# Optimization experiments

Hardware: AMD Instinct MI355X
Metric: run time of the kernel (lower is better)

The kernel has to match this reference:

```python
import jax, jax.numpy as jnp
import numpy as np

HEADS = 8
DIM_HEAD = 64
WINDOW = 128
PERSIST = 4
EPS = 1.1920929e-07  # torch nn.RMSNorm default eps = finfo(fp32).eps


def _rope_freqs(n, d, dtype):
    inv_freq = 1.0 / (10000.0 ** (jnp.arange(0, d, 2, dtype=jnp.float32) / d))
    freqs = jnp.arange(n, dtype=jnp.float32)[:, None] * inv_freq[None, :]  # [n, d/2]
    freqs = jnp.repeat(freqs, 2, axis=-1)  # interleaved repeat -> [n, d]
    return jnp.cos(freqs).astype(dtype), jnp.sin(freqs).astype(dtype)


def _rotate_half(x):
    # interleaved pairs (x0,x1),(x2,x3)... -> (-x1,x0),(-x3,x2)...
    x = x.reshape(*x.shape[:-1], -1, 2)
    x1, x2 = x[..., 0], x[..., 1]
    return jnp.stack((-x2, x1), axis=-1).reshape(*x.shape[:-2], -1)


def setup_inputs() -> dict:
    key = jax.random.key(0)
    k1, k2, k3 = jax.random.split(key, 3)
    B, N, D = 1, 4096, 1024
    dim_inner = HEADS * DIM_HEAD  # 512
    return {
        "seq": jax.random.normal(k1, (B, N, D), dtype=jnp.float32),
        "g": jnp.ones((D,), dtype=jnp.float32),
        "w_qkv": jax.random.normal(k2, (D, 3 * dim_inner), dtype=jnp.float32) * 0.02,
        "w_out": jax.random.normal(k3, (dim_inner, D), dtype=jnp.float32) * 0.02,
    }


def reference(seq, g, w_qkv, w_out):
    B, N, D = seq.shape
    H, Dh = HEADS, DIM_HEAD

    # RMSNorm
    x = seq * jax.lax.rsqrt(jnp.mean(seq * seq, axis=-1, keepdims=True) + EPS) * g

    # QKV projection -> [B, H, N, Dh]
    qkv = x @ w_qkv
    q, k, v = jnp.split(qkv, 3, axis=-1)
    to_heads = lambda t: t.reshape(B, N, H, Dh).transpose(0, 2, 1, 3)
    q, k, v = map(to_heads, (q, k, v))

    # rotary embeddings (same positions for q and k)
    cos, sin = _rope_freqs(N, Dh, q.dtype)
    q = q * cos + _rotate_half(q) * sin
    k = k * cos + _rotate_half(k) * sin

    # causal & (persist | sliding-window) mask
    idx = jnp.arange(N)
    dist = idx[:, None] - idx[None, :]
    mask = (dist >= 0) & ((idx[None, :] < PERSIST) | (dist <= WINDOW))  # [N, N]

    scale = Dh ** -0.5
    scores = jnp.einsum("bhid,bhjd->bhij", q, k) * scale
    neg = -jnp.finfo(scores.dtype).max
    scores = jnp.where(mask[None, None], scores, neg)
    attn = jax.nn.softmax(scores, axis=-1)
    out = jnp.einsum("bhij,bhjd->bhid", attn, v)

    out = out.transpose(0, 2, 1, 3).reshape(B, N, H * Dh)
    return out @ w_out
```

## Files before the change

kernel.cpp:

```cpp
#include <hip/hip_runtime.h>
#include <hip/hip_bf16.h>
#include <math.h>

#define SEQ    4096
#define DMODEL 1024
#define NHEADS 8
#define DH     64
#define DINNER 512
#define NQKV   1536
#define WINDOW 128
#define PERSIST 4
#define EPS 1.1920929e-07f

typedef unsigned short u16;
typedef unsigned int   u32;
typedef __bf16  bf16_8 __attribute__((ext_vector_type(8)));
typedef float   f32x4  __attribute__((ext_vector_type(4)));

union BV { bf16_8 v; u16 s[8]; };

__device__ __forceinline__ float b2f(u16 u) {
    union { u32 i; float f; } v; v.i = ((u32)u) << 16; return v.f;
}
__device__ __forceinline__ u16 f2b(float f) {
    union { float f; u32 i; } v; v.f = f;
    u32 i = v.i;
    u32 r = (i + 0x7fffu + ((i >> 16) & 1u)) >> 16;
    return (u16)r;
}

#define GLD16(gp, lp) __builtin_amdgcn_global_load_lds( \
    (const __attribute__((address_space(1))) void*)(gp), \
    (__attribute__((address_space(3))) void*)(lp), 16, 0, 0)

__device__ __forceinline__ void transpose_tile(const float* __restrict__ src,
                                               u16* __restrict__ dst,
                                               int K, int N, int bn, int bk,
                                               u16 (*t)[65], int tid) {
    int r = tid >> 4, c4 = (tid & 15) * 4;
    #pragma unroll
    for (int it = 0; it < 4; it++) {
        int row = r + it * 16;
        float4 v = *(const float4*)(src + (size_t)(bk + row) * N + bn + c4);
        t[row][c4 + 0] = f2b(v.x);
        t[row][c4 + 1] = f2b(v.y);
        t[row][c4 + 2] = f2b(v.z);
        t[row][c4 + 3] = f2b(v.w);
    }
    __syncthreads();
    #pragma unroll
    for (int it = 0; it < 4; it++) {
        int n = r + it * 16;
        u16* d = dst + (size_t)(bn + n) * K + bk + c4;
        d[0] = t[c4 + 0][n];
        d[1] = t[c4 + 1][n];
        d[2] = t[c4 + 2][n];
        d[3] = t[c4 + 3][n];
    }
}

__global__ __launch_bounds__(256) void prep_kernel(const float* __restrict__ wqkv,
                                                   const float* __restrict__ wout,
                                                   const float* __restrict__ seq,
                                                   const float* __restrict__ g,
                                                   u16* __restrict__ wqkv_bt,
                                                   u16* __restrict__ wout_bt,
                                                   u16* __restrict__ x) {
    __shared__ u16 t[64][65];
    __shared__ float wsum[4];
    int b = blockIdx.x, tid = threadIdx.x;
    if (b < 384) {
        transpose_tile(wqkv, wqkv_bt, DMODEL, NQKV, (b % 24) * 64, (b / 24) * 64, t, tid);
    } else if (b < 512) {
        int bb = b - 384;
        transpose_tile(wout, wout_bt, DINNER, DMODEL, (bb % 16) * 64, (bb / 16) * 64, t, tid);
    } else {
        int row = b - 512;
        float4 v = *(const float4*)(seq + (size_t)row * DMODEL + tid * 4);
        float ss = v.x*v.x + v.y*v.y + v.z*v.z + v.w*v.w;
        #pragma unroll
        for (int o = 32; o > 0; o >>= 1) ss += __shfl_xor(ss, o);
        if ((tid & 63) == 0) wsum[tid >> 6] = ss;
        __syncthreads();
        float tot = wsum[0] + wsum[1] + wsum[2] + wsum[3];
        float rstd = rsqrtf(tot * (1.0f / DMODEL) + EPS);
        float4 gv = *(const float4*)(g + tid * 4);
        uint2 o;
        o.x = (u32)f2b(v.x * rstd * gv.x) | ((u32)f2b(v.y * rstd * gv.y) << 16);
        o.y = (u32)f2b(v.z * rstd * gv.z) | ((u32)f2b(v.w * rstd * gv.w) << 16);
        *(uint2*)(x + (size_t)row * DMODEL + tid * 4) = o;
    }
}

template <int MODE>
__global__ __launch_bounds__(256, 2) void gemm2_kernel(const u16* __restrict__ A,
                                                       const u16* __restrict__ Bt,
                                                       u16* __restrict__ C0,
                                                       u16* __restrict__ C1,
                                                       u16* __restrict__ C2,
                                                       float* __restrict__ Cf,
                                                       int M, int N, int K) {
    __shared__ u16 As[128 * 64];
    __shared__ u16 Bs[128 * 64];
    int bx = blockIdx.x, by = blockIdx.y, tid = threadIdx.x;
    int lane = tid & 63, wave = tid >> 6;
    int m16 = lane & 15, quad = lane >> 4;
    int rw0 = (wave & 1) * 64, cw0 = (wave >> 1) * 64;

    f32x4 acc[4][4];
    #pragma unroll
    for (int mt = 0; mt < 4; mt++)
        #pragma unroll
        for (int nt = 0; nt < 4; nt++) acc[mt][nt] = (f32x4){0.f, 0.f, 0.f, 0.f};

    int lrow = lane & 7, lkc = lane >> 3;
    const u16* Ag = A  + (size_t)(by * 128 + lrow) * K + lkc * 8;
    const u16* Bg = Bt + (size_t)(bx * 128 + lrow) * K + lkc * 8;

    for (int k0 = 0; k0 < K; k0 += 64) {
        #pragma unroll
        for (int r = 0; r < 4; r++) {
            int gg = wave * 4 + r;
            GLD16(Ag + (size_t)(gg * 8) * K + k0, As + gg * 512);
            GLD16(Bg + (size_t)(gg * 8) * K + k0, Bs + gg * 512);
        }
        __syncthreads();

        #pragma unroll
        for (int kk = 0; kk < 2; kk++) {
            int kc = kk * 4 + quad;
            bf16_8 afr[4], bfr[4];
            #pragma unroll
            for (int mt = 0; mt < 4; mt++) {
                int row = rw0 + mt * 16 + m16;
                afr[mt] = *(const bf16_8*)(As + (row >> 3) * 512 + kc * 64 + (row & 7) * 8);
            }
            #pragma unroll
            for (int nt = 0; nt < 4; nt++) {
                int col = cw0 + nt * 16 + m16;
                bfr[nt] = *(const bf16_8*)(Bs + (col >> 3) * 512 + kc * 64 + (col & 7) * 8);
            }
            #pragma unroll
            for (int mt = 0; mt < 4; mt++)
                #pragma unroll
                for (int nt = 0; nt < 4; nt++)
                    acc[mt][nt] = __builtin_amdgcn_mfma_f32_16x16x32_bf16(afr[mt], bfr[nt], acc[mt][nt], 0, 0, 0);
        }
        __syncthreads();
    }

    #pragma unroll
    for (int nt = 0; nt < 4; nt++) {
        int col = bx * 128 + cw0 + nt * 16 + m16;
        if (MODE == 0) {
            int tt = (col & 63) >> 1;
            float inv = exp2f(-(float)(2 * tt) * (13.287712379549449f / 64.0f));
            bool isv = (col >= 2 * DINNER);
            bool odd = (col & 1);
            int tens = col >> 9, hh = (col >> 6) & 7, dh = col & 63;
            u16* dst = (tens == 0) ? C0 : ((tens == 1) ? C1 : C2);
            #pragma unroll
            for (int mt = 0; mt < 4; mt++) {
                #pragma unroll
                for (int r = 0; r < 4; r++) {
                    int row = by * 128 + rw0 + mt * 16 + quad * 4 + r;
                    float own = acc[mt][nt][r];
                    float part = __shfl_xor(own, 1);
                    float val = own;
                    if (!isv) {
                        float s, c;
                        __sincosf((float)row * inv, &s, &c);
                        val = odd ? (own * c + part * s) : (own * c - part * s);
                    }
                    dst[((size_t)hh * SEQ + row) * DH + dh] = f2b(val);
                }
            }
        } else {
            #pragma unroll
            for (int mt = 0; mt < 4; mt++) {
                #pragma unroll
                for (int r = 0; r < 4; r++) {
                    int row = by * 128 + rw0 + mt * 16 + quad * 4 + r;
                    Cf[(size_t)row * N + col] = acc[mt][nt][r];
                }
            }
        }
    }
}

#define AROWS 208
#define KLD   72
#define PLD   168
#define VLD   222

__global__ __launch_bounds__(256, 2) void attn_mfma(const u16* __restrict__ Q,
                                                    const u16* __restrict__ Kt,
                                                    const u16* __restrict__ V,
                                                    u16* __restrict__ O) {
    __shared__ __align__(16) char smem[29952 + 64 * VLD * 2];
    u16* Ks = (u16*)smem;
    u16* Ps = (u16*)smem;
    u16* Vt = (u16*)(smem + 29952);
    int i0 = blockIdx.x * 64, h = blockIdx.y;
    int tid = threadIdx.x, wave = tid >> 6, lane = tid & 63;
    int m16 = lane & 15, quad = lane >> 4;
    int smin = (i0 > WINDOW) ? i0 - WINDOW : 0;

    for (int idx = tid; idx < AROWS * 8; idx += 256) {
        int row = idx >> 3, c = idx & 7;
        int j = (row < 16) ? row : (smin + row - 16);
        size_t goff = ((size_t)h * SEQ + j) * DH + c * 8;
        *(bf16_8*)(Ks + row * KLD + c * 8) = *(const bf16_8*)(Kt + goff);
        union BV u; u.v = *(const bf16_8*)(V + goff);
        #pragma unroll
        for (int e = 0; e < 8; e++) Vt[(c * 8 + e) * VLD + row] = u.s[e];
    }

    int iw0 = i0 + wave * 16;
    int iq = iw0 + m16;
    const u16* qrow = Q + ((size_t)h * SEQ + iq) * DH;
    bf16_8 qa = *(const bf16_8*)(qrow + quad * 8);
    bf16_8 qb = *(const bf16_8*)(qrow + 32 + quad * 8);
    __syncthreads();

    int start_w = (iw0 > WINDOW) ? iw0 - WINDOW : 0;
    int Dw = start_w - smin;
    int tlast = 31 + iw0 - start_w;
    int nch = (tlast >> 4) + 1;
    int nk32 = (tlast >> 5) + 1;

    f32x4 S[10];
    #pragma unroll
    for (int c = 0; c < 10; c++) {
        if (c < nch) {
            int t = c * 16 + m16;
            int row = (c == 0) ? t : (t + Dw);
            const u16* kp = Ks + row * KLD;
            bf16_8 kb0 = *(const bf16_8*)(kp + quad * 8);
            bf16_8 kb1 = *(const bf16_8*)(kp + 32 + quad * 8);
            f32x4 s = (f32x4){0.f, 0.f, 0.f, 0.f};
            s = __builtin_amdgcn_mfma_f32_16x16x32_bf16(qa, kb0, s, 0, 0, 0);
            s = __builtin_amdgcn_mfma_f32_16x16x32_bf16(qb, kb1, s, 0, 0, 0);
            S[c] = s;
        }
    }
    __syncthreads();

    float mrow[4] = {-1e30f, -1e30f, -1e30f, -1e30f};
    #pragma unroll
    for (int c = 0; c < 10; c++) {
        if (c < nch) {
            int t = c * 16 + m16;
            int j = (c == 0) ? t : (start_w + t - 16);
            #pragma unroll
            for (int r = 0; r < 4; r++) {
                int i = iw0 + quad * 4 + r;
                bool valid = (c == 0) ? (j < PERSIST && j < start_w)
                                      : (j <= i && (i - j <= WINDOW || j < PERSIST));
                float sv = valid ? S[c][r] * 0.125f : -1e30f;
                S[c][r] = sv;
                mrow[r] = fmaxf(mrow[r], sv);
            }
        }
    }
    #pragma unroll
    for (int r = 0; r < 4; r++) {
        #pragma unroll
        for (int o = 1; o < 16; o <<= 1) mrow[r] = fmaxf(mrow[r], __shfl_xor(mrow[r], o));
    }
    float srow[4] = {0.f, 0.f, 0.f, 0.f};
    #pragma unroll
    for (int c = 0; c < 10; c++) {
        if (c < nch) {
            #pragma unroll
            for (int r = 0; r < 4; r++) {
                float p = expf(S[c][r] - mrow[r]);
                S[c][r] = p;
                srow[r] += p;
            }
        }
    }
    #pragma unroll
    for (int r = 0; r < 4; r++) {
        #pragma unroll
        for (int o = 1; o < 16; o <<= 1) srow[r] += __shfl_xor(srow[r], o);
    }

    u16* pw = Ps + wave * 16 * PLD;
    #pragma unroll
    for (int c = 0; c < 10; c++) {
        #pragma unroll
        for (int r = 0; r < 4; r++) {
            u16 val = (c < nch) ? f2b(S[c][r]) : (u16)0;
            pw[(quad * 4 + r) * PLD + c * 16 + m16] = val;
        }
    }

    f32x4 oacc[4];
    #pragma unroll
    for (int nt = 0; nt < 4; nt++) oacc[nt] = (f32x4){0.f, 0.f, 0.f, 0.f};
    #pragma unroll
    for (int c2 = 0; c2 < 5; c2++) {
        if (c2 < nk32) {
            bf16_8 af = *(const bf16_8*)(pw + m16 * PLD + c2 * 32 + quad * 8);
            int kbase = c2 * 32 + quad * 8;
            int rowb = (kbase < 16) ? kbase : (kbase + Dw);
            #pragma unroll
            for (int nt = 0; nt < 4; nt++) {
                int d = nt * 16 + m16;
                bf16_8 bv = *(const bf16_8*)(Vt + d * VLD + rowb);
                oacc[nt] = __builtin_amdgcn_mfma_f32_16x16x32_bf16(af, bv, oacc[nt], 0, 0, 0);
            }
        }
    }

    #pragma unroll
    for (int nt = 0; nt < 4; nt++) {
        #pragma unroll
        for (int r = 0; r < 4; r++) {
            int i = iw0 + quad * 4 + r;
            O[(size_t)i * DINNER + h * DH + nt * 16 + m16] = f2b(oacc[nt][r] / srow[r]);
        }
    }
}

extern "C" void kernel_launch(void* const* d_in, const int* in_sizes, int n_in,
                              void* d_out, int out_size, void* d_ws, size_t ws_size,
                              hipStream_t stream) {
    const float* seq  = (const float*)d_in[0];
    const float* g    = (const float*)d_in[1];
    const float* wqkv = (const float*)d_in[2];
    const float* wout = (const float*)d_in[3];
    float* out = (float*)d_out;

    char* ws = (char*)d_ws;
    u16* x       = (u16*)(ws);
    u16* q       = (u16*)(ws + 8ll  * 1024 * 1024);
    u16* k       = (u16*)(ws + 12ll * 1024 * 1024);
    u16* v       = (u16*)(ws + 16ll * 1024 * 1024);
    u16* att     = (u16*)(ws + 20ll * 1024 * 1024);
    u16* wqkv_bt = (u16*)(ws + 24ll * 1024 * 1024);
    u16* wout_bt = (u16*)(ws + 27ll * 1024 * 1024);

    prep_kernel<<<4608, 256, 0, stream>>>(wqkv, wout, seq, g, wqkv_bt, wout_bt, x);

    dim3 g1(NQKV / 128, SEQ / 128);
    gemm2_kernel<0><<<g1, 256, 0, stream>>>(x, wqkv_bt, q, k, v, nullptr, SEQ, NQKV, DMODEL);

    dim3 g2(SEQ / 64, NHEADS);
    attn_mfma<<<g2, 256, 0, stream>>>(q, k, v, att);

    dim3 g3(DMODEL / 128, SEQ / 128);
    gemm2_kernel<1><<<g3, 256, 0, stream>>>(att, wout_bt, nullptr, nullptr, nullptr, out, SEQ, DMODEL, DINNER);
}
```

Before: 146.6 us.

## Shrink GEMM N-tiles for more blocks, add setprio and fast exp in attention

Measured after the change: 141.0 us. 3.9% less time.

```diff
diff --git a/kernel.cpp b/kernel.cpp
--- a/kernel.cpp
+++ b/kernel.cpp
@@ -92,7 +92,7 @@
     }
 }
 
-template <int MODE>
+template <int MODE, int NTW>
 __global__ __launch_bounds__(256, 2) void gemm2_kernel(const u16* __restrict__ A,
                                                        const u16* __restrict__ Bt,
                                                        u16* __restrict__ C0,
@@ -100,28 +100,34 @@
                                                        u16* __restrict__ C2,
                                                        float* __restrict__ Cf,
                                                        int M, int N, int K) {
+    constexpr int BN  = NTW * 32;
+    constexpr int GPW = BN / 32;
     __shared__ u16 As[128 * 64];
-    __shared__ u16 Bs[128 * 64];
+    __shared__ u16 Bs[BN * 64];
     int bx = blockIdx.x, by = blockIdx.y, tid = threadIdx.x;
     int lane = tid & 63, wave = tid >> 6;
     int m16 = lane & 15, quad = lane >> 4;
-    int rw0 = (wave & 1) * 64, cw0 = (wave >> 1) * 64;
-
-    f32x4 acc[4][4];
+    int rw0 = (wave & 1) * 64, cw0 = (wave >> 1) * (NTW * 16);
+
+    f32x4 acc[4][NTW];
     #pragma unroll
     for (int mt = 0; mt < 4; mt++)
         #pragma unroll
-        for (int nt = 0; nt < 4; nt++) acc[mt][nt] = (f32x4){0.f, 0.f, 0.f, 0.f};
+        for (int nt = 0; nt < NTW; nt++) acc[mt][nt] = (f32x4){0.f, 0.f, 0.f, 0.f};
 
     int lrow = lane & 7, lkc = lane >> 3;
     const u16* Ag = A  + (size_t)(by * 128 + lrow) * K + lkc * 8;
-    const u16* Bg = Bt + (size_t)(bx * 128 + lrow) * K + lkc * 8;
+    const u16* Bg = Bt + (size_t)(bx * BN  + lrow) * K + lkc * 8;
 
     for (int k0 = 0; k0 < K; k0 += 64) {
         #pragma unroll
         for (int r = 0; r < 4; r++) {
             int gg = wave * 4 + r;
             GLD16(Ag + (size_t)(gg * 8) * K + k0, As + gg * 512);
+        }
+        #pragma unroll
+        for (int r = 0; r < GPW; r++) {
+            int gg = wave * GPW + r;
             GLD16(Bg + (size_t)(gg * 8) * K + k0, Bs + gg * 512);
         }
         __syncthreads();
@@ -129,29 +135,29 @@
         #pragma unroll
         for (int kk = 0; kk < 2; kk++) {
             int kc = kk * 4 + quad;
-            bf16_8 afr[4], bfr[4];
+            bf16_8 afr[4], bfr[NTW];
             #pragma unroll
             for (int mt = 0; mt < 4; mt++) {
                 int row = rw0 + mt * 16 + m16;
                 afr[mt] = *(const bf16_8*)(As + (row >> 3) * 512 + kc * 64 + (row & 7) * 8);
             }
             #pragma unroll
-            for (int nt = 0; nt < 4; nt++) {
+            for (int nt = 0; nt < NTW; nt++) {
                 int col = cw0 + nt * 16 + m16;
                 bfr[nt] = *(const bf16_8*)(Bs + (col >> 3) * 512 + kc * 64 + (col & 7) * 8);
             }
             #pragma unroll
             for (int mt = 0; mt < 4; mt++)
                 #pragma unroll
-                for (int nt = 0; nt < 4; nt++)
+                for (int nt = 0; nt < NTW; nt++)
                     acc[mt][nt] = __builtin_amdgcn_mfma_f32_16x16x32_bf16(afr[mt], bfr[nt], acc[mt][nt], 0, 0, 0);
         }
         __syncthreads();
     }
 
     #pragma unroll
-    for (int nt = 0; nt < 4; nt++) {
-        int col = bx * 128 + cw0 + nt * 16 + m16;
+    for (int nt = 0; nt < NTW; nt++) {
+        int col = bx * BN + cw0 + nt * 16 + m16;
         if (MODE == 0) {
             int tt = (col & 63) >> 1;
             float inv = exp2f(-(float)(2 * tt) * (13.287712379549449f / 64.0f));
@@ -230,6 +236,7 @@
     int nk32 = (tlast >> 5) + 1;
 
     f32x4 S[10];
+    __builtin_amdgcn_s_setprio(1);
     #pragma unroll
     for (int c = 0; c < 10; c++) {
         if (c < nch) {
@@ -244,6 +251,7 @@
             S[c] = s;
         }
     }
+    __builtin_amdgcn_s_setprio(0);
     __syncthreads();
 
     float mrow[4] = {-1e30f, -1e30f, -1e30f, -1e30f};
@@ -274,7 +282,7 @@
         if (c < nch) {
             #pragma unroll
             for (int r = 0; r < 4; r++) {
-                float p = expf(S[c][r] - mrow[r]);
+                float p = __expf(S[c][r] - mrow[r]);
                 S[c][r] = p;
                 srow[r] += p;
             }
@@ -299,6 +307,7 @@
     f32x4 oacc[4];
     #pragma unroll
     for (int nt = 0; nt < 4; nt++) oacc[nt] = (f32x4){0.f, 0.f, 0.f, 0.f};
+    __builtin_amdgcn_s_setprio(1);
     #pragma unroll
     for (int c2 = 0; c2 < 5; c2++) {
         if (c2 < nk32) {
@@ -313,13 +322,17 @@
             }
         }
     }
-
+    __builtin_amdgcn_s_setprio(0);
+
+    float rinv[4];
+    #pragma unroll
+    for (int r = 0; r < 4; r++) rinv[r] = 1.0f / srow[r];
     #pragma unroll
     for (int nt = 0; nt < 4; nt++) {
         #pragma unroll
         for (int r = 0; r < 4; r++) {
             int i = iw0 + quad * 4 + r;
-            O[(size_t)i * DINNER + h * DH + nt * 16 + m16] = f2b(oacc[nt][r] / srow[r]);
+            O[(size_t)i * DINNER + h * DH + nt * 16 + m16] = f2b(oacc[nt][r] * rinv[r]);
         }
     }
 }
@@ -344,12 +357,12 @@
 
     prep_kernel<<<4608, 256, 0, stream>>>(wqkv, wout, seq, g, wqkv_bt, wout_bt, x);
 
-    dim3 g1(NQKV / 128, SEQ / 128);
-    gemm2_kernel<0><<<g1, 256, 0, stream>>>(x, wqkv_bt, q, k, v, nullptr, SEQ, NQKV, DMODEL);
+    dim3 g1(NQKV / 96, SEQ / 128);
+    gemm2_kernel<0, 3><<<g1, 256, 0, stream>>>(x, wqkv_bt, q, k, v, nullptr, SEQ, NQKV, DMODEL);
 
     dim3 g2(SEQ / 64, NHEADS);
     attn_mfma<<<g2, 256, 0, stream>>>(q, k, v, att);
 
-    dim3 g3(DMODEL / 128, SEQ / 128);
-    gemm2_kernel<1><<<g3, 256, 0, stream>>>(att, wout_bt, nullptr, nullptr, nullptr, out, SEQ, DMODEL, DINNER);
-}
+    dim3 g3(DMODEL / 64, SEQ / 128);
+    gemm2_kernel<1, 2><<<g3, 256, 0, stream>>>(att, wout_bt, nullptr, nullptr, nullptr, out, SEQ, DMODEL, DINNER);
+}
```
